# Optimization experiments

Hardware: AMD Instinct MI355X
Metric: run time of the kernel (lower is better)

## Reference

```python
import jax, jax.numpy as jnp
import numpy as np

NEG = -1e9  # max-semiring 'zero' / structural mask value


def _cky_max(pot, lengths):
    """Max-plus CKY inside pass (torch_struct CKY_CRF with MaxSemiring).

    pot: [B, N, N] label-maxed span potentials, pot[b, i, j] = score of span (i, j).
    Returns [B] best binary-tree score for each sequence of given length.
    betaA[b, i, w]      = best score of span starting at i with width w (span [i, i+w]).
    betaB[b, j, N-1-w]  = best score of span ending at j with width w.
    """
    B, N, _ = pot.shape
    term = jnp.diagonal(pot, axis1=1, axis2=2)  # [B, N] width-0 spans
    betaA = jnp.full((B, N, N), NEG, dtype=pot.dtype).at[:, :, 0].set(term)
    betaB = jnp.full((B, N, N), NEG, dtype=pot.dtype).at[:, :, N - 1].set(term)
    for w in range(1, N):
        Y = betaA[:, : N - w, :w]       # [B, N-w, w] left children, widths 0..w-1
        Z = betaB[:, w:, N - w:]        # [B, N-w, w] right children (matching splits)
        span = jnp.diagonal(pot, offset=w, axis1=1, axis2=2)  # [B, N-w] pot[b, i, i+w]
        new = jnp.max(Y + Z, axis=-1) + span
        betaA = betaA.at[:, : N - w, w].set(new)
        betaB = betaB.at[:, w:, N - w - 1].set(new)
    final = betaA[:, 0, :]  # [B, N]: final[b, l-1] = best tree over [0, l-1]
    return final[jnp.arange(B), lengths - 1]


def setup_inputs() -> dict:
    key = jax.random.key(0)
    k1, k2 = jax.random.split(key)
    B, N, L = 64, 128, 32
    logits = jax.random.normal(k1, (B, N, N, L), dtype=jnp.float32)
    labels = jax.random.randint(k2, (B, N, N), 0, L, dtype=jnp.int64)
    return {"logits": logits, "labels": labels}


def reference(logits, labels):
    B, N, _, L = logits.shape
    gold_event = jax.nn.one_hot(jnp.maximum(labels, 0), L, dtype=logits.dtype)
    logits = logits - logits[..., :1]
    lengths = jnp.sum(labels[:, 0, :] != -100, axis=-1)
    augment = 1.0 - gold_event
    # force_root_constituent=True: forbid non-constituent root span
    augment = augment.at[jnp.arange(B), 0, lengths - 1, 0].add(-1e9)
    pot = jnp.max(logits + augment, axis=-1)  # max-semiring sum over label dim
    pred_score = _cky_max(pot, lengths)                      # [B]
    gold_score = jnp.sum(logits * gold_event, axis=(1, 2, 3))  # [B]
    margin_losses = jax.nn.relu(pred_score - gold_score)
    return jnp.mean(margin_losses)
```

## Files before the change

kernel.cpp:

```cpp
#include <hip/hip_runtime.h>

#define BATCH 64
#define SEQ   128
#define NLAB  32
#define NEGF  -3.0e38f

__global__ __launch_bounds__(256) void pot_gold_kernel(
    const float* __restrict__ logits, const int* __restrict__ labels,
    float* __restrict__ pot, float* __restrict__ gpart)
{
    const int tid = threadIdx.x;
    const int wave = tid >> 6, lane = tid & 63;
    __shared__ __align__(16) float LP[4 * 16 * 36];
    __shared__ float gred[4];
    __shared__ int s_len;
    float* W = LP + wave * (16 * 36);

    const int block_cell0 = blockIdx.x * 256;
    const int b = block_cell0 >> 14;
    const bool has_row0 = (blockIdx.x & 63) == 0;

    if (has_row0 && tid < 64) {
        const size_t base = (size_t)b << 14;
        int cnt = (labels[base + tid] != -100) + (labels[base + 64 + tid] != -100);
        #pragma unroll
        for (int d = 32; d; d >>= 1) cnt += __shfl_down(cnt, d, 64);
        if (tid == 0) s_len = cnt;
    }
    __syncthreads();
    const int len = has_row0 ? s_len : -1;

    float gacc = 0.0f;
    const int wave_cell0 = block_cell0 + wave * 64;

    #pragma unroll
    for (int chunk = 0; chunk < 4; ++chunk) {
        const int c0 = wave_cell0 + chunk * 16;
        const float4* src = reinterpret_cast<const float4*>(logits) + ((size_t)c0 << 3);
        const float4 f0 = src[lane];
        const float4 f1 = src[lane + 64];
        const int lv = (lane < 16) ? labels[c0 + lane] : 0;

        {
            const int cA = lane >> 3, tA = lane & 7;
            *reinterpret_cast<float4*>(W + cA * 36 + tA * 4) = f0;
            const int q1 = lane + 64;
            const int cB = q1 >> 3, tB = q1 & 7;
            *reinterpret_cast<float4*>(W + cB * 36 + tB * 4) = f1;
        }
        const int c = lane >> 2, u = lane & 3;
        const float4 r0 = *reinterpret_cast<const float4*>(W + c * 36 + u * 8);
        const float4 r1 = *reinterpret_cast<const float4*>(W + c * 36 + u * 8 + 4);

        int lab = __shfl(lv, c, 64);
        if (lab < 0) lab = 0;
        const float l0 = __shfl(r0.x, c << 2, 64);

        const int cell = c0 + c;
        const int ci = (cell >> 7) & (SEQ - 1);
        const int cj = cell & (SEQ - 1);
        const bool special = (ci == 0) && (cj == len - 1);

        const float vv[8] = { r0.x, r0.y, r0.z, r0.w, r1.x, r1.y, r1.z, r1.w };
        float m = NEGF, g = 0.0f;
        #pragma unroll
        for (int e = 0; e < 8; ++e) {
            const int l = u * 8 + e;
            const float r = vv[e] - l0;
            const bool isg = (l == lab);
            g = isg ? r : g;
            float cand = r + (isg ? 0.0f : 1.0f);
            if (l == 0 && special) cand -= 1.0e9f;
            m = fmaxf(m, cand);
        }
        m = fmaxf(m, __shfl_xor(m, 1, 64));
        m = fmaxf(m, __shfl_xor(m, 2, 64));
        g += __shfl_xor(g, 1, 64);
        g += __shfl_xor(g, 2, 64);
        if (u == 0) {
            pot[cell] = m;
            gacc += g;
        }
    }

    #pragma unroll
    for (int d = 1; d < 64; d <<= 1) gacc += __shfl_xor(gacc, d, 64);
    if (lane == 0) gred[wave] = gacc;
    __syncthreads();
    if (tid == 0)
        gpart[blockIdx.x] = gred[0] + gred[1] + gred[2] + gred[3];
}

template<int S>
__device__ __forceinline__ void cky_step(
    float* __restrict__ A, float* __restrict__ Bt, const int wn,
    const int i, const int s, float& pre_m, float& val, float& potv,
    float& awB, const float a0)
{
    const int iw = i + wn;
    if (iw < SEQ) {
        const float newB = Bt[iw * 132 + (SEQ - wn)];
        const float m = fmaxf(pre_m, fmaxf(a0 + newB, val + awB));
        val = m + potv;
        if (s == 0) {
            A[i * 132 + wn] = val;
            Bt[iw * 132 + (SEQ - 1 - wn)] = val;
        }
    }
    if (iw + 1 < SEQ) {
        const float* Arow = A + i * 132;
        potv = Arow[wn + 1];
        const float* Brow = Bt + (iw + 1) * 132 + (SEQ - wn - 1);
        awB = Brow[wn];
        const int kmax = wn - 1;
        float pm = NEGF;
        #pragma unroll 2
        for (int q = s; (q << 2) <= kmax; q += 4) {
            const int k0 = q << 2;
            float4 a = *reinterpret_cast<const float4*>(Arow + k0);
            const float* bp = Brow + k0;
            float b0, b1, b2, b3;
            if (S == 0) {
                const float4 bv = *reinterpret_cast<const float4*>(bp);
                b0 = bv.x; b1 = bv.y; b2 = bv.z; b3 = bv.w;
            } else if (S == 2) {
                const float2 u0 = *reinterpret_cast<const float2*>(bp);
                const float2 u1 = *reinterpret_cast<const float2*>(bp + 2);
                b0 = u0.x; b1 = u0.y; b2 = u1.x; b3 = u1.y;
            } else {
                b0 = bp[0];
                const float2 u = *reinterpret_cast<const float2*>(bp + 1);
                b1 = u.x; b2 = u.y;
                b3 = bp[3];
            }
            a.x = (k0 != 0)        ? a.x : NEGF;
            a.y = (k0 + 1 <= kmax) ? a.y : NEGF;
            a.z = (k0 + 2 <= kmax) ? a.z : NEGF;
            a.w = (k0 + 3 <= kmax) ? a.w : NEGF;
            pm = fmaxf(pm, fmaxf(fmaxf(a.x + b0, a.y + b1),
                                 fmaxf(a.z + b2, a.w + b3)));
        }
        pm = fmaxf(pm, __shfl_xor(pm, 1, 4));
        pm = fmaxf(pm, __shfl_xor(pm, 2, 4));
        pre_m = pm;
    } else {
        pre_m = NEGF;
    }
    __syncthreads();
}

__global__ __launch_bounds__(512, 1) void cky_kernel(
    const float* __restrict__ pot, const float* __restrict__ gpart,
    const int* __restrict__ labels, float* __restrict__ out)
{
    const int b = blockIdx.x;
    const int tid = threadIdx.x;
    const float* p = pot + (size_t)b * SEQ * SEQ;

    __shared__ __align__(16) float A[SEQ * 132];
    __shared__ __align__(16) float Bt[SEQ * 132];
    __shared__ int s_len;
    __shared__ float s_gold;

    if (tid < 64) {
        const size_t base = (size_t)b << 14;
        int cnt = (labels[base + tid] != -100) + (labels[base + 64 + tid] != -100);
        #pragma unroll
        for (int d = 32; d; d >>= 1) cnt += __shfl_down(cnt, d, 64);
        if (tid == 0) s_len = cnt;
    } else if (tid < 128) {
        float g = gpart[b * 64 + (tid - 64)];
        #pragma unroll
        for (int d = 32; d; d >>= 1) g += __shfl_down(g, d, 64);
        if (tid == 64) s_gold = g;
    }

    {
        const float4 neg4 = make_float4(NEGF, NEGF, NEGF, NEGF);
        float4* a4 = reinterpret_cast<float4*>(A);
        float4* b4 = reinterpret_cast<float4*>(Bt);
        for (int idx = tid; idx < SEQ * 132 / 4; idx += 512) {
            a4[idx] = neg4; b4[idx] = neg4;
        }
    }
    __syncthreads();
    {
        const float4* p4 = reinterpret_cast<const float4*>(p);
        for (int qi = tid; qi < SEQ * SEQ / 4; qi += 512) {
            const int i = qi >> 5;
            const int j0 = (qi & 31) << 2;
            const float4 v = p4[qi];
            const float vv[4] = { v.x, v.y, v.z, v.w };
            #pragma unroll
            for (int c2 = 0; c2 < 4; ++c2) {
                const int j = j0 + c2;
                if (j >= i) {
                    A[i * 132 + (j - i)] = vv[c2];
                    Bt[j * 132 + (SEQ - 1 - (j - i))] = vv[c2];
                }
            }
        }
    }
    __syncthreads();

    const int i = tid >> 2, s = tid & 3;
    float pre_m = NEGF, val = 0.0f, potv = 0.0f, awB = 0.0f, a0 = 0.0f;
    if (i + 1 < SEQ) {
        const float* Arow = A + i * 132;
        a0   = Arow[0];
        val  = a0;
        potv = Arow[1];
        awB  = Bt[(i + 1) * 132 + (SEQ - 1)];
    }

    int wn = 1;
    #pragma unroll 1
    for (int ph = 0; ph < 31; ++ph) {
        cky_step<2>(A, Bt, wn,     i, s, pre_m, val, potv, awB, a0);
        cky_step<1>(A, Bt, wn + 1, i, s, pre_m, val, potv, awB, a0);
        cky_step<0>(A, Bt, wn + 2, i, s, pre_m, val, potv, awB, a0);
        cky_step<3>(A, Bt, wn + 3, i, s, pre_m, val, potv, awB, a0);
        wn += 4;
    }
    cky_step<2>(A, Bt, 125, i, s, pre_m, val, potv, awB, a0);
    cky_step<1>(A, Bt, 126, i, s, pre_m, val, potv, awB, a0);
    cky_step<0>(A, Bt, 127, i, s, pre_m, val, potv, awB, a0);

    if (tid == 0) {
        const int len = s_len;
        const float pred = A[len - 1];
        const float margin = fmaxf(pred - s_gold, 0.0f);
        atomicAdd(out, margin * (1.0f / (float)BATCH));
    }
}

extern "C" void kernel_launch(void* const* d_in, const int* in_sizes, int n_in,
                              void* d_out, int out_size, void* d_ws, size_t ws_size,
                              hipStream_t stream) {
    const float* logits = (const float*)d_in[0];
    const int* labels = (const int*)d_in[1];
    float* out = (float*)d_out;

    float* pot = (float*)d_ws;
    float* gpart = pot + (size_t)BATCH * SEQ * SEQ;

    (void)hipMemsetAsync(out, 0, sizeof(float), stream);

    pot_gold_kernel<<<BATCH * SEQ * SEQ / 256, 256, 0, stream>>>(
        logits, labels, pot, gpart);
    cky_kernel<<<BATCH, 512, 0, stream>>>(pot, gpart, labels, out);
}
```

Measured before the change: 279.2 us.

## Block CKY inside pass into width tiles of 16 with register-held diagonal band

Restructures the CKY recurrence so each group of 16 widths first computes the bulk split maxima over already-finished widths in one batched pass, reusing each loaded A chunk across 16 target widths. Only the intra-tile dependent splits are then resolved sequentially, using register-held recent values (av, alo), which shortens the per-step work between barriers. It also drops the NEG initialization of shared buffers, relying on all read entries being written first. This costs many more registers (several 16-element arrays), which risks spills.

```diff
diff --git a/kernel.cpp b/kernel.cpp
--- a/kernel.cpp
+++ b/kernel.cpp
@@ -4,6 +4,7 @@
 #define SEQ   128
 #define NLAB  32
 #define NEGF  -3.0e38f
+#define PA    132
 
 __global__ __launch_bounds__(256) void pot_gold_kernel(
     const float* __restrict__ logits, const int* __restrict__ labels,
@@ -91,64 +92,6 @@
         gpart[blockIdx.x] = gred[0] + gred[1] + gred[2] + gred[3];
 }
 
-template<int S>
-__device__ __forceinline__ void cky_step(
-    float* __restrict__ A, float* __restrict__ Bt, const int wn,
-    const int i, const int s, float& pre_m, float& val, float& potv,
-    float& awB, const float a0)
-{
-    const int iw = i + wn;
-    if (iw < SEQ) {
-        const float newB = Bt[iw * 132 + (SEQ - wn)];
-        const float m = fmaxf(pre_m, fmaxf(a0 + newB, val + awB));
-        val = m + potv;
-        if (s == 0) {
-            A[i * 132 + wn] = val;
-            Bt[iw * 132 + (SEQ - 1 - wn)] = val;
-        }
-    }
-    if (iw + 1 < SEQ) {
-        const float* Arow = A + i * 132;
-        potv = Arow[wn + 1];
-        const float* Brow = Bt + (iw + 1) * 132 + (SEQ - wn - 1);
-        awB = Brow[wn];
-        const int kmax = wn - 1;
-        float pm = NEGF;
-        #pragma unroll 2
-        for (int q = s; (q << 2) <= kmax; q += 4) {
-            const int k0 = q << 2;
-            float4 a = *reinterpret_cast<const float4*>(Arow + k0);
-            const float* bp = Brow + k0;
-            float b0, b1, b2, b3;
-            if (S == 0) {
-                const float4 bv = *reinterpret_cast<const float4*>(bp);
-                b0 = bv.x; b1 = bv.y; b2 = bv.z; b3 = bv.w;
-            } else if (S == 2) {
-                const float2 u0 = *reinterpret_cast<const float2*>(bp);
-                const float2 u1 = *reinterpret_cast<const float2*>(bp + 2);
-                b0 = u0.x; b1 = u0.y; b2 = u1.x; b3 = u1.y;
-            } else {
-                b0 = bp[0];
-                const float2 u = *reinterpret_cast<const float2*>(bp + 1);
-                b1 = u.x; b2 = u.y;
-                b3 = bp[3];
-            }
-            a.x = (k0 != 0)        ? a.x : NEGF;
-            a.y = (k0 + 1 <= kmax) ? a.y : NEGF;
-            a.z = (k0 + 2 <= kmax) ? a.z : NEGF;
-            a.w = (k0 + 3 <= kmax) ? a.w : NEGF;
-            pm = fmaxf(pm, fmaxf(fmaxf(a.x + b0, a.y + b1),
-                                 fmaxf(a.z + b2, a.w + b3)));
-        }
-        pm = fmaxf(pm, __shfl_xor(pm, 1, 4));
-        pm = fmaxf(pm, __shfl_xor(pm, 2, 4));
-        pre_m = pm;
-    } else {
-        pre_m = NEGF;
-    }
-    __syncthreads();
-}
-
 __global__ __launch_bounds__(512, 1) void cky_kernel(
     const float* __restrict__ pot, const float* __restrict__ gpart,
     const int* __restrict__ labels, float* __restrict__ out)
@@ -157,8 +100,8 @@
     const int tid = threadIdx.x;
     const float* p = pot + (size_t)b * SEQ * SEQ;
 
-    __shared__ __align__(16) float A[SEQ * 132];
-    __shared__ __align__(16) float Bt[SEQ * 132];
+    __shared__ __align__(16) float A[SEQ * PA];
+    __shared__ __align__(16) float Bt[SEQ * PA];
     __shared__ int s_len;
     __shared__ float s_gold;
 
@@ -175,15 +118,6 @@
         if (tid == 64) s_gold = g;
     }
 
-    {
-        const float4 neg4 = make_float4(NEGF, NEGF, NEGF, NEGF);
-        float4* a4 = reinterpret_cast<float4*>(A);
-        float4* b4 = reinterpret_cast<float4*>(Bt);
-        for (int idx = tid; idx < SEQ * 132 / 4; idx += 512) {
-            a4[idx] = neg4; b4[idx] = neg4;
-        }
-    }
-    __syncthreads();
     {
         const float4* p4 = reinterpret_cast<const float4*>(p);
         for (int qi = tid; qi < SEQ * SEQ / 4; qi += 512) {
@@ -195,8 +129,8 @@
             for (int c2 = 0; c2 < 4; ++c2) {
                 const int j = j0 + c2;
                 if (j >= i) {
-                    A[i * 132 + (j - i)] = vv[c2];
-                    Bt[j * 132 + (SEQ - 1 - (j - i))] = vv[c2];
+                    A[i * PA + (j - i)] = vv[c2];
+                    Bt[j * PA + (SEQ - 1 - (j - i))] = vv[c2];
                 }
             }
         }
@@ -204,27 +138,145 @@
     __syncthreads();
 
     const int i = tid >> 2, s = tid & 3;
-    float pre_m = NEGF, val = 0.0f, potv = 0.0f, awB = 0.0f, a0 = 0.0f;
-    if (i + 1 < SEQ) {
-        const float* Arow = A + i * 132;
-        a0   = Arow[0];
-        val  = a0;
-        potv = Arow[1];
-        awB  = Bt[(i + 1) * 132 + (SEQ - 1)];
-    }
-
-    int wn = 1;
-    #pragma unroll 1
-    for (int ph = 0; ph < 31; ++ph) {
-        cky_step<2>(A, Bt, wn,     i, s, pre_m, val, potv, awB, a0);
-        cky_step<1>(A, Bt, wn + 1, i, s, pre_m, val, potv, awB, a0);
-        cky_step<0>(A, Bt, wn + 2, i, s, pre_m, val, potv, awB, a0);
-        cky_step<3>(A, Bt, wn + 3, i, s, pre_m, val, potv, awB, a0);
-        wn += 4;
-    }
-    cky_step<2>(A, Bt, 125, i, s, pre_m, val, potv, awB, a0);
-    cky_step<1>(A, Bt, 126, i, s, pre_m, val, potv, awB, a0);
-    cky_step<0>(A, Bt, 127, i, s, pre_m, val, potv, awB, a0);
+    float alo[16], av[16], pv[16], md[16];
+
+    #pragma unroll
+    for (int t = 0; t < 4; ++t) {
+        const float4 v = *reinterpret_cast<const float4*>(&A[i * PA + 4 * t]);
+        pv[4*t] = v.x; pv[4*t+1] = v.y; pv[4*t+2] = v.z; pv[4*t+3] = v.w;
+    }
+    av[0] = pv[0];
+    #pragma unroll
+    for (int d = 1; d < 16; ++d) {
+        const int j = i + d;
+        if (j < SEQ) {
+            float bo[16];
+            const int NQ = (d + 3) >> 2;
+            #pragma unroll
+            for (int t = 0; t < NQ; ++t) {
+                const float4 v = *reinterpret_cast<const float4*>(&Bt[j * PA + 124 - 4 * t]);
+                bo[4*t] = v.w; bo[4*t+1] = v.z; bo[4*t+2] = v.y; bo[4*t+3] = v.x;
+            }
+            float val = NEGF;
+            #pragma unroll
+            for (int m = 0; m < d; ++m)
+                val = fmaxf(val, av[d - 1 - m] + bo[m]);
+            val += pv[d];
+            av[d] = val;
+            if (s == 0) {
+                A[i * PA + d] = val;
+                Bt[j * PA + (SEQ - 1 - d)] = val;
+            }
+        }
+        __syncthreads();
+    }
+    #pragma unroll
+    for (int k = 0; k < 16; ++k) alo[k] = av[k];
+
+    for (int W = 16; W < SEQ; W += 16) {
+        #pragma unroll
+        for (int t = 0; t < 4; ++t) {
+            const float4 v = *reinterpret_cast<const float4*>(&A[i * PA + W + 4 * t]);
+            pv[4*t] = v.x; pv[4*t+1] = v.y; pv[4*t+2] = v.z; pv[4*t+3] = v.w;
+        }
+        #pragma unroll
+        for (int d = 0; d < 16; ++d) md[d] = NEGF;
+
+        {
+            const int k0 = s << 2;
+            const float4 a = *reinterpret_cast<const float4*>(&A[i * PA + k0]);
+            const float aa[4] = { a.x, a.y, a.z, a.w };
+            #pragma unroll
+            for (int d = 0; d < 16; ++d) {
+                const int j = i + W + d;
+                if (j < SEQ) {
+                    const float* bp = &Bt[j * PA + (SEQ - W - d) + k0];
+                    float b0, b1, b2, b3;
+                    if ((d & 3) == 0) {
+                        const float4 v = *reinterpret_cast<const float4*>(bp);
+                        b0 = v.x; b1 = v.y; b2 = v.z; b3 = v.w;
+                    } else if ((d & 3) == 2) {
+                        const float2 v0 = *reinterpret_cast<const float2*>(bp);
+                        const float2 v1 = *reinterpret_cast<const float2*>(bp + 2);
+                        b0 = v0.x; b1 = v0.y; b2 = v1.x; b3 = v1.y;
+                    } else {
+                        b0 = bp[0];
+                        const float2 v = *reinterpret_cast<const float2*>(bp + 1);
+                        b1 = v.x; b2 = v.y; b3 = bp[3];
+                    }
+                    const float a0 = (k0 + 0 >= d) ? aa[0] : NEGF;
+                    const float a1 = (k0 + 1 >= d) ? aa[1] : NEGF;
+                    const float a2 = (k0 + 2 >= d) ? aa[2] : NEGF;
+                    const float a3 = (k0 + 3 >= d) ? aa[3] : NEGF;
+                    md[d] = fmaxf(md[d], fmaxf(fmaxf(a0 + b0, a1 + b1),
+                                               fmaxf(a2 + b2, a3 + b3)));
+                }
+            }
+        }
+        for (int q = s + 4; q < (W >> 2); q += 4) {
+            const int k0 = q << 2;
+            const float4 a = *reinterpret_cast<const float4*>(&A[i * PA + k0]);
+            #pragma unroll
+            for (int d = 0; d < 16; ++d) {
+                const int j = i + W + d;
+                if (j < SEQ) {
+                    const float* bp = &Bt[j * PA + (SEQ - W - d) + k0];
+                    float b0, b1, b2, b3;
+                    if ((d & 3) == 0) {
+                        const float4 v = *reinterpret_cast<const float4*>(bp);
+                        b0 = v.x; b1 = v.y; b2 = v.z; b3 = v.w;
+                    } else if ((d & 3) == 2) {
+                        const float2 v0 = *reinterpret_cast<const float2*>(bp);
+                        const float2 v1 = *reinterpret_cast<const float2*>(bp + 2);
+                        b0 = v0.x; b1 = v0.y; b2 = v1.x; b3 = v1.y;
+                    } else {
+                        b0 = bp[0];
+                        const float2 v = *reinterpret_cast<const float2*>(bp + 1);
+                        b1 = v.x; b2 = v.y; b3 = bp[3];
+                    }
+                    md[d] = fmaxf(md[d], fmaxf(fmaxf(a.x + b0, a.y + b1),
+                                               fmaxf(a.z + b2, a.w + b3)));
+                }
+            }
+        }
+        #pragma unroll
+        for (int d = 0; d < 16; ++d) {
+            md[d] = fmaxf(md[d], __shfl_xor(md[d], 1, 4));
+            md[d] = fmaxf(md[d], __shfl_xor(md[d], 2, 4));
+        }
+
+        #pragma unroll
+        for (int d = 0; d < 16; ++d) {
+            const int w = W + d;
+            const int j = i + w;
+            if (j < SEQ) {
+                float val = md[d];
+                if (d > 0) {
+                    float bo[16], bf[16];
+                    const int NQ = (d + 3) >> 2;
+                    #pragma unroll
+                    for (int t = 0; t < NQ; ++t) {
+                        const float4 v = *reinterpret_cast<const float4*>(&Bt[j * PA + 124 - 4 * t]);
+                        bo[4*t] = v.w; bo[4*t+1] = v.z; bo[4*t+2] = v.y; bo[4*t+3] = v.x;
+                        const float4 u = *reinterpret_cast<const float4*>(&Bt[j * PA + 124 - W - 4 * t]);
+                        bf[4*t] = u.w; bf[4*t+1] = u.z; bf[4*t+2] = u.y; bf[4*t+3] = u.x;
+                    }
+                    #pragma unroll
+                    for (int m = 0; m < d; ++m) {
+                        val = fmaxf(val, av[d - 1 - m] + bo[m]);
+                        val = fmaxf(val, alo[d - 1 - m] + bf[m]);
+                    }
+                }
+                val += pv[d];
+                av[d] = val;
+                if (s == 0) {
+                    A[i * PA + w] = val;
+                    Bt[j * PA + (SEQ - 1 - w)] = val;
+                }
+            }
+            __syncthreads();
+        }
+    }
 
     if (tid == 0) {
         const int len = s_len;
```

Result: faster. 259.7 us (-7.0%).
